# Optimization experiments

Hardware: AMD Instinct MI355X
Metric: run time of the kernel (lower is better)

## Reference

```python
import jax, jax.numpy as jnp
import numpy as np

G, FO, FI = 8, 64, 64   # n_group, fo, fi
N_ITER = 3
B, H, W = 32, 64, 64


def setup_inputs() -> dict:
    key = jax.random.key(0)
    k1, k2, k3 = jax.random.split(key, 3)
    x = jax.random.normal(k1, (B, G * FI, H, W), jnp.float32)
    # kaiming_normal on [fo*g, fi, 1, 1] -> std = sqrt(2/fi); stored as [g, fo, fi]
    weight = jax.random.normal(k2, (G, FO, FI), jnp.float32) * np.float32(np.sqrt(2.0 / FI))
    bias = jax.random.normal(k3, (FO,), jnp.float32)
    return {"x": x, "weight": weight, "bias": bias}


def reference(x, weight, bias):
    b, c, h, w = x.shape
    g, fo, fi = weight.shape
    # grouped 1x1 conv: split channels into g groups of fi, contract each with its [fo, fi] block
    xr = x.reshape(b, g, fi, h, w)
    con = jnp.einsum('bgihw,goi->bgohw', xr, weight)  # [B, g, fo, H, W]
    beta = jnp.zeros((1, g, 1, 1, 1), dtype=x.dtype)
    for i in range(N_ITER):
        alpha = jax.nn.sigmoid(beta)
        v = jnp.sum(alpha * con, axis=1, keepdims=True)      # [B, 1, fo, H, W]
        if i == N_ITER - 1:
            return v[:, 0] + bias[None, :, None, None]       # [B, fo, H, W]
        beta = beta + jnp.sum(v * con, axis=2, keepdims=True)  # [B, g, 1, H, W]
```

## Files before the change

kernel.cpp:

```cpp
#include <hip/hip_runtime.h>


#define NG 8
#define NFO 64
#define NFI 64
#define NB 32
#define NH 64
#define NW 64
#define HW (NH * NW)

typedef float v2f __attribute__((ext_vector_type(2)));

__device__ __forceinline__ void stage_piece(const float* gsrc, float* ldst) {
    __builtin_amdgcn_global_load_lds(
        (const __attribute__((address_space(1))) void*)gsrc,
        (__attribute__((address_space(3))) void*)ldst, 16, 0, 0);
}

__global__ __launch_bounds__(256, 8) void conv_kernel(
    const float* __restrict__ x, const float* __restrict__ weight,
    float* __restrict__ con)
{
    const int tid = threadIdx.x;
    const int p = tid & 63;
    const int q = __builtin_amdgcn_readfirstlane(tid >> 6);

    const int id = blockIdx.x;
    const int t = id & 63;
    const int g = (id >> 6) & 7;
    const int b = id >> 9;

    __shared__ __align__(16) float smem[4096];

    const float* xg = x + ((size_t)b * (NG * NFI) + (size_t)g * NFI) * HW + t * 64;

#pragma unroll
    for (int cc = 0; cc < 4; ++cc) {
        const int chb = q * 16 + cc * 4;
        stage_piece(xg + (size_t)(chb + (p >> 4)) * HW + (p & 15) * 4,
                    smem + chb * 64);
    }
    asm volatile("s_waitcnt vmcnt(0)" ::: "memory");
    __builtin_amdgcn_s_barrier();

    v2f acc[16];
#pragma unroll
    for (int f = 0; f < 16; ++f) acc[f] = (v2f){0.f, 0.f};

    const float* wq = weight + ((size_t)g * NFO + (size_t)q * 16) * NFI;
#pragma unroll
    for (int ib = 0; ib < 8; ++ib) {
        v2f xq[4];
#pragma unroll
        for (int j = 0; j < 4; ++j) {
            xq[j].x = smem[(ib * 8 + 2 * j) * 64 + p];
            xq[j].y = smem[(ib * 8 + 2 * j + 1) * 64 + p];
        }
#pragma unroll
        for (int f = 0; f < 16; ++f) {
            const float* wr = wq + (size_t)f * NFI + ib * 8;
#pragma unroll
            for (int j = 0; j < 4; ++j) {
                const v2f wv = *(const v2f*)(wr + 2 * j);
                acc[f] = __builtin_elementwise_fma(wv, xq[j], acc[f]);
            }
        }
    }

    float* crow = con + (((size_t)(b * NG + g) * NFO + (size_t)q * 16)) * HW
                      + t * 64 + p;
#pragma unroll
    for (int f = 0; f < 16; ++f)
        crow[(size_t)f * HW] = acc[f].x + acc[f].y;
}

__global__ __launch_bounds__(256) void route_kernel(
    const float* __restrict__ con, const float* __restrict__ bias,
    float* __restrict__ out)
{
    const int tid = threadIdx.x;
    const int p = tid & 63;
    const int q = __builtin_amdgcn_readfirstlane(tid >> 6);

    const int id = blockIdx.x;
    const int t = id & 63;
    const int b = id >> 6;

    __shared__ float pbuf[4][8][64];
    __shared__ float alphaS[8][64];
    __shared__ float betaS[8][64];

    float c[8][16];
#pragma unroll
    for (int g = 0; g < 8; ++g) {
        const float* cr = con + (((size_t)(b * NG + g) * NFO + (size_t)q * 16)) * HW
                              + t * 64 + p;
#pragma unroll
        for (int f = 0; f < 16; ++f) c[g][f] = cr[(size_t)f * HW];
    }

    float v[16];

#pragma unroll
    for (int f = 0; f < 16; ++f) {
        float s = c[0][f];
#pragma unroll
        for (int g = 1; g < 8; ++g) s += c[g][f];
        v[f] = 0.5f * s;
    }
#pragma unroll
    for (int g = 0; g < 8; ++g) {
        float s = 0.f;
#pragma unroll
        for (int f = 0; f < 16; ++f) s = fmaf(v[f], c[g][f], s);
        pbuf[q][g][p] = s;
    }
    __syncthreads();
    for (int k = tid; k < 512; k += 256) {
        const int gg = k >> 6, pp = k & 63;
        const float bs = pbuf[0][gg][pp] + pbuf[1][gg][pp] +
                         pbuf[2][gg][pp] + pbuf[3][gg][pp];
        betaS[gg][pp] = bs;
        alphaS[gg][pp] = 1.f / (1.f + __expf(-bs));
    }
    __syncthreads();

    float a[8];
#pragma unroll
    for (int g = 0; g < 8; ++g) a[g] = alphaS[g][p];
#pragma unroll
    for (int f = 0; f < 16; ++f) {
        float s = 0.f;
#pragma unroll
        for (int g = 0; g < 8; ++g) s = fmaf(a[g], c[g][f], s);
        v[f] = s;
    }
#pragma unroll
    for (int g = 0; g < 8; ++g) {
        float s = 0.f;
#pragma unroll
        for (int f = 0; f < 16; ++f) s = fmaf(v[f], c[g][f], s);
        pbuf[q][g][p] = s;
    }
    __syncthreads();
    for (int k = tid; k < 512; k += 256) {
        const int gg = k >> 6, pp = k & 63;
        const float bs = betaS[gg][pp] +
                         pbuf[0][gg][pp] + pbuf[1][gg][pp] +
                         pbuf[2][gg][pp] + pbuf[3][gg][pp];
        alphaS[gg][pp] = 1.f / (1.f + __expf(-bs));
    }
    __syncthreads();

#pragma unroll
    for (int g = 0; g < 8; ++g) a[g] = alphaS[g][p];

    const float* bq = bias + q * 16;
    float* orow = out + (((size_t)b * NFO + (size_t)q * 16) * NH + t) * NW + p;
#pragma unroll
    for (int f = 0; f < 16; ++f) {
        float s = bq[f];
#pragma unroll
        for (int g = 0; g < 8; ++g) s = fmaf(a[g], c[g][f], s);
        orow[(size_t)f * HW] = s;
    }
}

__global__ __launch_bounds__(256) void dynrout_kernel(
    const float* __restrict__ x, const float* __restrict__ weight,
    const float* __restrict__ bias, float* __restrict__ out)
{
    const int tid = threadIdx.x;
    const int p = tid & 63;
    const int q = __builtin_amdgcn_readfirstlane(tid >> 6);

    const int wg = blockIdx.x;
    const int b = wg >> 6;
    const int h = wg & 63;

    __shared__ __align__(16) float smem[6144];

    const float* xrow = x + (size_t)b * (NG * NFI) * HW + (size_t)h * NW;
    const float* gpiece = xrow + (size_t)(p >> 4) * HW + (size_t)(p & 15) * 4;

    float con[8][16];
#pragma unroll
    for (int g = 0; g < 8; ++g)
#pragma unroll
        for (int f = 0; f < 16; ++f) con[g][f] = 0.f;

#pragma unroll
    for (int cc = 0; cc < 2; ++cc) {
        float* dst = smem + cc * 2048;
        const float* g0 = gpiece + (size_t)(cc * 32) * HW;
        stage_piece(g0 + (size_t)(q * 8) * HW,     dst + (q * 2) * 256);
        stage_piece(g0 + (size_t)(q * 8 + 4) * HW, dst + (q * 2 + 1) * 256);
    }

#pragma unroll
    for (int c = 0; c < 16; ++c) {
        if (c < 15) asm volatile("s_waitcnt vmcnt(2)" ::: "memory");
        else        asm volatile("s_waitcnt vmcnt(0)" ::: "memory");
        __builtin_amdgcn_s_barrier();

        if (c < 14) {
            float* dst = smem + ((c + 2) % 3) * 2048;
            const float* g0 = gpiece + (size_t)((c + 2) * 32) * HW;
            stage_piece(g0 + (size_t)(q * 8) * HW,     dst + (q * 2) * 256);
            stage_piece(g0 + (size_t)(q * 8 + 4) * HW, dst + (q * 2 + 1) * 256);
        }

        const int g = c >> 1;
        const float* bufp = smem + (c % 3) * 2048;

        v2f xp[16];
#pragma unroll
        for (int jp = 0; jp < 16; ++jp) {
            xp[jp].x = bufp[(2 * jp) * 64 + p];
            xp[jp].y = bufp[(2 * jp + 1) * 64 + p];
        }

        const float* wq = weight + ((size_t)g * NFO + (size_t)q * 16) * NFI + (c & 1) * 32;
#pragma unroll
        for (int f = 0; f < 16; ++f) {
            const float* wr = wq + (size_t)f * NFI;
            v2f a0 = {0.f, 0.f}, a1 = {0.f, 0.f};
#pragma unroll
            for (int jp = 0; jp < 16; jp += 2) {
                const v2f w0 = *(const v2f*)(wr + 2 * jp);
                const v2f w1 = *(const v2f*)(wr + 2 * jp + 2);
                a0 = __builtin_elementwise_fma(w0, xp[jp], a0);
                a1 = __builtin_elementwise_fma(w1, xp[jp + 1], a1);
            }
            con[g][f] += (a0.x + a1.x) + (a0.y + a1.y);
        }
    }
    __syncthreads();

    float* pbuf   = smem;
    float* alphaS = smem + 2048;
    float* betaS  = smem + 2560;

    float v[16];
#pragma unroll
    for (int f = 0; f < 16; ++f) {
        float s = con[0][f];
#pragma unroll
        for (int g = 1; g < 8; ++g) s += con[g][f];
        v[f] = 0.5f * s;
    }
#pragma unroll
    for (int g = 0; g < 8; ++g) {
        float s = 0.f;
#pragma unroll
        for (int f = 0; f < 16; ++f) s = fmaf(v[f], con[g][f], s);
        pbuf[(q * 8 + g) * 64 + p] = s;
    }
    __syncthreads();
    for (int k = tid; k < 512; k += 256) {
        const int gg = k >> 6, pp = k & 63;
        const float bs = pbuf[gg * 64 + pp] + pbuf[512 + gg * 64 + pp] +
                         pbuf[1024 + gg * 64 + pp] + pbuf[1536 + gg * 64 + pp];
        betaS[gg * 64 + pp] = bs;
        alphaS[gg * 64 + pp] = 1.f / (1.f + __expf(-bs));
    }
    __syncthreads();

    float a[8];
#pragma unroll
    for (int g = 0; g < 8; ++g) a[g] = alphaS[g * 64 + p];
#pragma unroll
    for (int f = 0; f < 16; ++f) {
        float s = 0.f;
#pragma unroll
        for (int g = 0; g < 8; ++g) s = fmaf(a[g], con[g][f], s);
        v[f] = s;
    }
#pragma unroll
    for (int g = 0; g < 8; ++g) {
        float s = 0.f;
#pragma unroll
        for (int f = 0; f < 16; ++f) s = fmaf(v[f], con[g][f], s);
        pbuf[(q * 8 + g) * 64 + p] = s;
    }
    __syncthreads();
    for (int k = tid; k < 512; k += 256) {
        const int gg = k >> 6, pp = k & 63;
        const float bs = betaS[gg * 64 + pp] +
                         pbuf[gg * 64 + pp] + pbuf[512 + gg * 64 + pp] +
                         pbuf[1024 + gg * 64 + pp] + pbuf[1536 + gg * 64 + pp];
        alphaS[gg * 64 + pp] = 1.f / (1.f + __expf(-bs));
    }
    __syncthreads();

#pragma unroll
    for (int g = 0; g < 8; ++g) a[g] = alphaS[g * 64 + p];

    const float* bq = bias + q * 16;
    float* orow = out + (((size_t)b * NFO + (size_t)q * 16) * NH + h) * NW + p;
#pragma unroll
    for (int f = 0; f < 16; ++f) {
        float s = bq[f];
#pragma unroll
        for (int g = 0; g < 8; ++g) s = fmaf(a[g], con[g][f], s);
        orow[(size_t)f * HW] = s;
    }
}

extern "C" void kernel_launch(void* const* d_in, const int* in_sizes, int n_in,
                              void* d_out, int out_size, void* d_ws, size_t ws_size,
                              hipStream_t stream) {
    const float* x      = (const float*)d_in[0];
    const float* weight = (const float*)d_in[1];
    const float* bias   = (const float*)d_in[2];
    float* out = (float*)d_out;

    const size_t need = (size_t)NB * NG * NFO * HW * sizeof(float);
    if (d_ws != nullptr && ws_size >= need) {
        float* con = (float*)d_ws;
        conv_kernel<<<dim3(NB * NG * 64), dim3(256), 0, stream>>>(x, weight, con);
        route_kernel<<<dim3(NB * 64), dim3(256), 0, stream>>>(con, bias, out);
    } else {
        dynrout_kernel<<<dim3(NB * NH), dim3(256), 0, stream>>>(x, weight, bias, out);
    }
}
```

Measured before the change: 491.3 us.

## Load conv input column directly into registers instead of LDS staging

The conv kernel drops the LDS staging of the 64-channel input tile and the barrier that went with it. Each thread now loads all 64 input channels for its pixel straight from global memory into 64 registers, then loops over its 16 output channels using two accumulators. The 8-waves occupancy hint is removed to allow the higher register count. The cost is that each of the 4 waves in a block reloads the same x tile from global memory (a 4x redundant read served by cache) and occupancy may drop.

Result: slower. 502.1 us (+2.2%).

```diff
diff --git a/kernel.cpp b/kernel.cpp
--- a/kernel.cpp
+++ b/kernel.cpp
@@ -17,7 +17,7 @@
         (__attribute__((address_space(3))) void*)ldst, 16, 0, 0);
 }
 
-__global__ __launch_bounds__(256, 8) void conv_kernel(
+__global__ __launch_bounds__(256) void conv_kernel(
     const float* __restrict__ x, const float* __restrict__ weight,
     float* __restrict__ con)
 {
@@ -30,48 +30,33 @@
     const int g = (id >> 6) & 7;
     const int b = id >> 9;
 
-    __shared__ __align__(16) float smem[4096];
-
-    const float* xg = x + ((size_t)b * (NG * NFI) + (size_t)g * NFI) * HW + t * 64;
-
-#pragma unroll
-    for (int cc = 0; cc < 4; ++cc) {
-        const int chb = q * 16 + cc * 4;
-        stage_piece(xg + (size_t)(chb + (p >> 4)) * HW + (p & 15) * 4,
-                    smem + chb * 64);
-    }
-    asm volatile("s_waitcnt vmcnt(0)" ::: "memory");
-    __builtin_amdgcn_s_barrier();
-
-    v2f acc[16];
-#pragma unroll
-    for (int f = 0; f < 16; ++f) acc[f] = (v2f){0.f, 0.f};
+    const float* xcol = x + ((size_t)b * (NG * NFI) + (size_t)g * NFI) * HW
+                          + t * 64 + p;
+
+    v2f xr[32];
+#pragma unroll
+    for (int c2 = 0; c2 < 32; ++c2) {
+        xr[c2].x = xcol[(size_t)(2 * c2) * HW];
+        xr[c2].y = xcol[(size_t)(2 * c2 + 1) * HW];
+    }
 
     const float* wq = weight + ((size_t)g * NFO + (size_t)q * 16) * NFI;
-#pragma unroll
-    for (int ib = 0; ib < 8; ++ib) {
-        v2f xq[4];
-#pragma unroll
-        for (int j = 0; j < 4; ++j) {
-            xq[j].x = smem[(ib * 8 + 2 * j) * 64 + p];
-            xq[j].y = smem[(ib * 8 + 2 * j + 1) * 64 + p];
-        }
-#pragma unroll
-        for (int f = 0; f < 16; ++f) {
-            const float* wr = wq + (size_t)f * NFI + ib * 8;
-#pragma unroll
-            for (int j = 0; j < 4; ++j) {
-                const v2f wv = *(const v2f*)(wr + 2 * j);
-                acc[f] = __builtin_elementwise_fma(wv, xq[j], acc[f]);
-            }
-        }
-    }
-
     float* crow = con + (((size_t)(b * NG + g) * NFO + (size_t)q * 16)) * HW
                       + t * 64 + p;
-#pragma unroll
-    for (int f = 0; f < 16; ++f)
-        crow[(size_t)f * HW] = acc[f].x + acc[f].y;
+
+#pragma unroll
+    for (int f = 0; f < 16; ++f) {
+        const float* wr = wq + (size_t)f * NFI;
+        v2f a0 = {0.f, 0.f}, a1 = {0.f, 0.f};
+#pragma unroll
+        for (int c2 = 0; c2 < 32; c2 += 2) {
+            const v2f w0 = *(const v2f*)(wr + 2 * c2);
+            const v2f w1 = *(const v2f*)(wr + 2 * c2 + 2);
+            a0 = __builtin_elementwise_fma(w0, xr[c2], a0);
+            a1 = __builtin_elementwise_fma(w1, xr[c2 + 1], a1);
+        }
+        crow[(size_t)f * HW] = (a0.x + a1.x) + (a0.y + a1.y);
+    }
 }
 
 __global__ __launch_bounds__(256) void route_kernel(
```
